# Kernel optimization log

Hardware: AMD Instinct MI355X
Metric: run time of the kernel (lower is better)

The kernel has to match this reference:

```python
import jax, jax.numpy as jnp
import numpy as np

N = 100000
F_IN = 128
HID = 128
E = 1600000


def gcn_conv(x, W, b, src, dst, dinv):
    # PyG GCNConv: h = x @ W; out_i = sum_j norm_ij * h_j (incl. self-loop) + b
    h = x @ W  # [N, H]
    norm = dinv[src] * dinv[dst]  # [E]
    msg = h[src] * norm[:, None]  # [E, H]
    agg = jax.ops.segment_sum(msg, dst, num_segments=N)
    agg = agg + h * (dinv * dinv)[:, None]  # self-loop contribution
    return agg + b


def setup_inputs() -> dict:
    key = jax.random.key(0)
    k1, k2, k3, k4, k5 = jax.random.split(key, 5)
    x = jax.random.normal(k1, (N, F_IN), dtype=jnp.float32)
    edge_index = jax.random.randint(k2, (2, E), 0, N, dtype=jnp.int64)
    s = 1.0 / np.sqrt(F_IN)
    W1 = jax.random.normal(k3, (F_IN, HID), dtype=jnp.float32) * s
    b1 = jnp.zeros((HID,), dtype=jnp.float32)
    sh = 1.0 / np.sqrt(HID)
    W2 = jax.random.normal(k4, (HID, HID), dtype=jnp.float32) * sh
    b2 = jnp.zeros((HID,), dtype=jnp.float32)
    Wfc = jax.random.normal(k5, (HID, 2), dtype=jnp.float32) * sh
    bfc = jnp.zeros((2,), dtype=jnp.float32)
    return {"x": x, "edge_index": edge_index, "W1": W1, "b1": b1,
            "W2": W2, "b2": b2, "Wfc": Wfc, "bfc": bfc}


def reference(x, edge_index, W1, b1, W2, b2, Wfc, bfc):
    src, dst = edge_index[0], edge_index[1]
    # degree with self-loops (edge weight 1), computed on target nodes
    deg = jax.ops.segment_sum(jnp.ones((E,), jnp.float32), dst, num_segments=N) + 1.0
    dinv = jax.lax.rsqrt(deg)
    h = jax.nn.relu(gcn_conv(x, W1, b1, src, dst, dinv))
    h = jax.nn.relu(gcn_conv(h, W2, b2, src, dst, dinv))
    logits = h @ Wfc + bfc  # [N, 2]
    return jax.nn.log_softmax(logits, axis=1)
```

## Files before the change

kernel.cpp:

```cpp
#include <hip/hip_runtime.h>
#include <math.h>

#define N_NODES 100000
#define FDIM 128
#define E_EDGES 1600000
#define NSCAN_BLKS ((N_NODES + 1023) / 1024)
#define NPASS 8
#define PASS_NODES 12500

typedef unsigned short bf16_t;
typedef __attribute__((ext_vector_type(8))) short short8;
typedef __attribute__((ext_vector_type(4))) float f32x4;

__device__ inline bf16_t f2bf(float f) {
    unsigned int u = __float_as_uint(f);
    return (bf16_t)((u + 0x7fffu + ((u >> 16) & 1u)) >> 16);
}
__device__ inline float2 bfpair(unsigned int u) {
    return make_float2(__uint_as_float(u << 16), __uint_as_float(u & 0xffff0000u));
}

__global__ __launch_bounds__(256) void hist_kernel(const int* __restrict__ dst,
                                                   int* __restrict__ cnt) {
    int pass = blockIdx.x & (NPASS - 1);
    int e = (blockIdx.x >> 3) * 256 + threadIdx.x;
    if (e >= E_EDGES) return;
    int d = dst[e];
    if ((unsigned)(d - pass * PASS_NODES) < (unsigned)PASS_NODES)
        atomicAdd(&cnt[d], 1);
}

__global__ __launch_bounds__(256) void scan1(const int* __restrict__ cnt,
                                             int* __restrict__ excl,
                                             int* __restrict__ bsum) {
    __shared__ int lds[256];
    const int b = blockIdx.x, t = threadIdx.x;
    const int base = b * 1024 + t * 4;
    int v[4];
#pragma unroll
    for (int q = 0; q < 4; ++q) {
        int i = base + q;
        v[q] = (i < N_NODES) ? cnt[i] : 0;
    }
    int tsum = v[0] + v[1] + v[2] + v[3];
    lds[t] = tsum;
    __syncthreads();
    for (int off = 1; off < 256; off <<= 1) {
        int x = lds[t];
        int y = (t >= off) ? lds[t - off] : 0;
        __syncthreads();
        lds[t] = x + y;
        __syncthreads();
    }
    int texcl = lds[t] - tsum;
    if (t == 255) bsum[b] = lds[t];
    int run = texcl;
#pragma unroll
    for (int q = 0; q < 4; ++q) {
        int i = base + q;
        if (i < N_NODES) excl[i] = run;
        run += v[q];
    }
}

__global__ __launch_bounds__(128) void scan2(int* __restrict__ bsum) {
    __shared__ int lds[128];
    const int t = threadIdx.x;
    int v = (t < NSCAN_BLKS) ? bsum[t] : 0;
    lds[t] = v;
    __syncthreads();
    for (int off = 1; off < 128; off <<= 1) {
        int x = lds[t];
        int y = (t >= off) ? lds[t - off] : 0;
        __syncthreads();
        lds[t] = x + y;
        __syncthreads();
    }
    if (t < NSCAN_BLKS) bsum[t] = lds[t] - v;
}

__global__ __launch_bounds__(256) void scan3(int* __restrict__ rowptr,
                                             const int* __restrict__ bsum,
                                             const int* __restrict__ cnt,
                                             float* __restrict__ dinv) {
    int i = blockIdx.x * blockDim.x + threadIdx.x;
    if (i < N_NODES) {
        rowptr[i] += bsum[i >> 10];
        dinv[i] = rsqrtf((float)cnt[i] + 1.0f);
    }
    if (i == 0) rowptr[N_NODES] = E_EDGES;
}

__global__ __launch_bounds__(256) void scatter_kernel(const int* __restrict__ src,
                                                      const int* __restrict__ dst,
                                                      const int* __restrict__ rowptr,
                                                      const float* __restrict__ dinv,
                                                      int* __restrict__ cursor,
                                                      int2* __restrict__ emeta) {
    int pass = blockIdx.x & (NPASS - 1);
    int e = (blockIdx.x >> 3) * 256 + threadIdx.x;
    if (e >= E_EDGES) return;
    int d = dst[e];
    if ((unsigned)(d - pass * PASS_NODES) < (unsigned)PASS_NODES) {
        int s = src[e];
        int p = rowptr[d] + atomicAdd(&cursor[d], 1);
        float nrm = dinv[s] * dinv[d];
        emeta[p] = make_int2(s, __float_as_int(nrm));
    }
}

__global__ __launch_bounds__(256) void wcvt_kernel(const float* __restrict__ W,
                                                   bf16_t* __restrict__ Wt) {
    int idx = blockIdx.x * 256 + threadIdx.x;
    int k = idx >> 7, c = idx & 127;
    Wt[c * 128 + k] = f2bf(W[idx]);
}

template <bool A_IS_F32>
__global__ __launch_bounds__(256) void gemm_mfma(const void* __restrict__ Aptr,
                                                 const bf16_t* __restrict__ Wt,
                                                 bf16_t* __restrict__ H) {
    const int tid = threadIdx.x;
    const int wave = tid >> 6;
    const int l = tid & 63;
    const int r = l & 15;
    const int g = l >> 4;
    const int row0 = (blockIdx.x * 4 + wave) * 16;
    const int arow = min(row0 + r, N_NODES - 1);

    f32x4 acc[8];
#pragma unroll
    for (int ct = 0; ct < 8; ++ct) acc[ct] = (f32x4){0.f, 0.f, 0.f, 0.f};

#pragma unroll
    for (int ks = 0; ks < 4; ++ks) {
        const int kbase = ks * 32 + g * 8;
        short8 a;
        if constexpr (A_IS_F32) {
            const float* X = (const float*)Aptr;
            const float4 x0 = *((const float4*)(X + (size_t)arow * 128 + kbase));
            const float4 x1 = *((const float4*)(X + (size_t)arow * 128 + kbase + 4));
            a[0] = (short)f2bf(x0.x); a[1] = (short)f2bf(x0.y);
            a[2] = (short)f2bf(x0.z); a[3] = (short)f2bf(x0.w);
            a[4] = (short)f2bf(x1.x); a[5] = (short)f2bf(x1.y);
            a[6] = (short)f2bf(x1.z); a[7] = (short)f2bf(x1.w);
        } else {
            const bf16_t* X = (const bf16_t*)Aptr;
            a = *((const short8*)(X + (size_t)arow * 128 + kbase));
        }
#pragma unroll
        for (int ct = 0; ct < 8; ++ct) {
            short8 b = *((const short8*)(Wt + (ct * 16 + r) * 128 + kbase));
            acc[ct] = __builtin_amdgcn_mfma_f32_16x16x32_bf16(a, b, acc[ct], 0, 0, 0);
        }
    }

#pragma unroll
    for (int j = 0; j < 4; ++j) {
        const int row = row0 + g * 4 + j;
        if (row < N_NODES) {
            bf16_t* hp = H + (size_t)row * 128 + r;
#pragma unroll
            for (int ct = 0; ct < 8; ++ct) hp[ct * 16] = f2bf(acc[ct][j]);
        }
    }
}

__global__ __launch_bounds__(256) void agg_kernel(const int* __restrict__ rowptr,
                                                  const int2* __restrict__ emeta,
                                                  const float* __restrict__ dinv,
                                                  const bf16_t* __restrict__ h,
                                                  const float* __restrict__ bias,
                                                  bf16_t* __restrict__ out) {
    int gid = blockIdx.x * blockDim.x + threadIdx.x;
    int node = gid >> 6;
    int lane = gid & 63;
    if (node >= N_NODES) return;
    float dd = dinv[node];
    float2 v = bfpair(((const unsigned*)(h + (size_t)node * 128))[lane]);
    float sc = dd * dd;
    float accx = v.x * sc, accy = v.y * sc;
    int j = rowptr[node];
    const int end = rowptr[node + 1];
    for (; j + 3 < end; j += 4) {
        int2 m0 = emeta[j], m1 = emeta[j + 1], m2 = emeta[j + 2], m3 = emeta[j + 3];
        float n0 = __int_as_float(m0.y), n1 = __int_as_float(m1.y);
        float n2 = __int_as_float(m2.y), n3 = __int_as_float(m3.y);
        float2 v0 = bfpair(((const unsigned*)(h + (size_t)m0.x * 128))[lane]);
        float2 v1 = bfpair(((const unsigned*)(h + (size_t)m1.x * 128))[lane]);
        float2 v2 = bfpair(((const unsigned*)(h + (size_t)m2.x * 128))[lane]);
        float2 v3 = bfpair(((const unsigned*)(h + (size_t)m3.x * 128))[lane]);
        accx += v0.x * n0 + v1.x * n1 + v2.x * n2 + v3.x * n3;
        accy += v0.y * n0 + v1.y * n1 + v2.y * n2 + v3.y * n3;
    }
    for (; j < end; ++j) {
        int2 m0 = emeta[j];
        float n0 = __int_as_float(m0.y);
        float2 v0 = bfpair(((const unsigned*)(h + (size_t)m0.x * 128))[lane]);
        accx += v0.x * n0;
        accy += v0.y * n0;
    }
    float2 b = ((const float2*)bias)[lane];
    accx = fmaxf(accx + b.x, 0.f);
    accy = fmaxf(accy + b.y, 0.f);
    unsigned o = (unsigned)f2bf(accx) | ((unsigned)f2bf(accy) << 16);
    ((unsigned*)(out + (size_t)node * 128))[lane] = o;
}

__global__ __launch_bounds__(256) void agg_fc_kernel(const int* __restrict__ rowptr,
                                                     const int2* __restrict__ emeta,
                                                     const float* __restrict__ dinv,
                                                     const bf16_t* __restrict__ h,
                                                     const float* __restrict__ bias,
                                                     const float* __restrict__ Wfc,
                                                     const float* __restrict__ bfc,
                                                     float* __restrict__ out) {
    int gid = blockIdx.x * blockDim.x + threadIdx.x;
    int node = gid >> 6;
    int lane = gid & 63;
    if (node >= N_NODES) return;
    float dd = dinv[node];
    float2 v = bfpair(((const unsigned*)(h + (size_t)node * 128))[lane]);
    float sc = dd * dd;
    float accx = v.x * sc, accy = v.y * sc;
    int j = rowptr[node];
    const int end = rowptr[node + 1];
    for (; j + 3 < end; j += 4) {
        int2 m0 = emeta[j], m1 = emeta[j + 1], m2 = emeta[j + 2], m3 = emeta[j + 3];
        float n0 = __int_as_float(m0.y), n1 = __int_as_float(m1.y);
        float n2 = __int_as_float(m2.y), n3 = __int_as_float(m3.y);
        float2 v0 = bfpair(((const unsigned*)(h + (size_t)m0.x * 128))[lane]);
        float2 v1 = bfpair(((const unsigned*)(h + (size_t)m1.x * 128))[lane]);
        float2 v2 = bfpair(((const unsigned*)(h + (size_t)m2.x * 128))[lane]);
        float2 v3 = bfpair(((const unsigned*)(h + (size_t)m3.x * 128))[lane]);
        accx += v0.x * n0 + v1.x * n1 + v2.x * n2 + v3.x * n3;
        accy += v0.y * n0 + v1.y * n1 + v2.y * n2 + v3.y * n3;
    }
    for (; j < end; ++j) {
        int2 m0 = emeta[j];
        float n0 = __int_as_float(m0.y);
        float2 v0 = bfpair(((const unsigned*)(h + (size_t)m0.x * 128))[lane]);
        accx += v0.x * n0;
        accy += v0.y * n0;
    }
    float2 b = ((const float2*)bias)[lane];
    accx = fmaxf(accx + b.x, 0.f);
    accy = fmaxf(accy + b.y, 0.f);
    int k0 = lane * 2;
    float a0 = accx * Wfc[k0 * 2 + 0] + accy * Wfc[(k0 + 1) * 2 + 0];
    float a1 = accx * Wfc[k0 * 2 + 1] + accy * Wfc[(k0 + 1) * 2 + 1];
#pragma unroll
    for (int off = 32; off > 0; off >>= 1) {
        a0 += __shfl_down(a0, off);
        a1 += __shfl_down(a1, off);
    }
    if (lane == 0) {
        float l0 = a0 + bfc[0];
        float l1 = a1 + bfc[1];
        float m = fmaxf(l0, l1);
        float lse = m + logf(expf(l0 - m) + expf(l1 - m));
        out[(size_t)node * 2 + 0] = l0 - lse;
        out[(size_t)node * 2 + 1] = l1 - lse;
    }
}

extern "C" void kernel_launch(void* const* d_in, const int* in_sizes, int n_in,
                              void* d_out, int out_size, void* d_ws, size_t ws_size,
                              hipStream_t stream) {
    const float* x   = (const float*)d_in[0];
    const int*   ei  = (const int*)d_in[1];
    const float* W1  = (const float*)d_in[2];
    const float* b1  = (const float*)d_in[3];
    const float* W2  = (const float*)d_in[4];
    const float* b2  = (const float*)d_in[5];
    const float* Wfc = (const float*)d_in[6];
    const float* bfc = (const float*)d_in[7];
    float* out = (float*)d_out;

    const int* src = ei;
    const int* dst = ei + E_EDGES;

    char* wp = (char*)d_ws;
    auto carve = [&](size_t bytes) -> char* {
        char* p = wp;
        wp += (bytes + 255) & ~(size_t)255;
        return p;
    };
    int*    cnt    = (int*)carve(N_NODES * 4);
    int*    rowptr = (int*)carve((N_NODES + 1) * 4);
    int*    cursor = (int*)carve(N_NODES * 4);
    int*    bsum   = (int*)carve(128 * 4);
    int2*   emeta  = (int2*)carve((size_t)E_EDGES * 8);
    float*  dinv   = (float*)carve(N_NODES * 4);
    bf16_t* hbuf   = (bf16_t*)carve((size_t)N_NODES * FDIM * 2);
    bf16_t* x2buf  = (bf16_t*)carve((size_t)N_NODES * FDIM * 2);
    bf16_t* Wt1    = (bf16_t*)carve(128 * 128 * 2);
    bf16_t* Wt2    = (bf16_t*)carve(128 * 128 * 2);

    const int NN_BLK = (N_NODES + 255) / 256;
    const int NODE_WAVE_BLK = (N_NODES * 64 + 255) / 256;
    const int EDGE_PASS_BLK = ((E_EDGES + 255) / 256) * NPASS;
    const int GEMM_BLK = (N_NODES + 63) / 64;

    hipMemsetAsync(cnt, 0, N_NODES * sizeof(int), stream);
    hipMemsetAsync(cursor, 0, N_NODES * sizeof(int), stream);
    hist_kernel<<<EDGE_PASS_BLK, 256, 0, stream>>>(dst, cnt);
    scan1<<<NSCAN_BLKS, 256, 0, stream>>>(cnt, rowptr, bsum);
    scan2<<<1, 128, 0, stream>>>(bsum);
    scan3<<<NN_BLK, 256, 0, stream>>>(rowptr, bsum, cnt, dinv);
    scatter_kernel<<<EDGE_PASS_BLK, 256, 0, stream>>>(src, dst, rowptr, dinv,
                                                      cursor, emeta);

    wcvt_kernel<<<64, 256, 0, stream>>>(W1, Wt1);
    wcvt_kernel<<<64, 256, 0, stream>>>(W2, Wt2);

    gemm_mfma<true><<<GEMM_BLK, 256, 0, stream>>>(x, Wt1, hbuf);
    agg_kernel<<<NODE_WAVE_BLK, 256, 0, stream>>>(rowptr, emeta, dinv, hbuf, b1, x2buf);

    gemm_mfma<false><<<GEMM_BLK, 256, 0, stream>>>(x2buf, Wt2, hbuf);
    agg_fc_kernel<<<NODE_WAVE_BLK, 256, 0, stream>>>(rowptr, emeta, dinv, hbuf, b2,
                                                     Wfc, bfc, out);
}
```

Baseline: 470.2 us.

## Prefetch edge metadata in aggregation, double GEMM rows per wave, merge small launches

```diff
diff --git a/kernel.cpp b/kernel.cpp
--- a/kernel.cpp
+++ b/kernel.cpp
@@ -82,11 +82,13 @@
 __global__ __launch_bounds__(256) void scan3(int* __restrict__ rowptr,
                                              const int* __restrict__ bsum,
                                              const int* __restrict__ cnt,
-                                             float* __restrict__ dinv) {
+                                             float* __restrict__ dinv,
+                                             int* __restrict__ cursor) {
     int i = blockIdx.x * blockDim.x + threadIdx.x;
     if (i < N_NODES) {
         rowptr[i] += bsum[i >> 10];
         dinv[i] = rsqrtf((float)cnt[i] + 1.0f);
+        cursor[i] = 0;
     }
     if (i == 0) rowptr[N_NODES] = E_EDGES;
 }
@@ -109,9 +111,14 @@
     }
 }
 
-__global__ __launch_bounds__(256) void wcvt_kernel(const float* __restrict__ W,
-                                                   bf16_t* __restrict__ Wt) {
-    int idx = blockIdx.x * 256 + threadIdx.x;
+__global__ __launch_bounds__(256) void wcvt_kernel(const float* __restrict__ W1,
+                                                   bf16_t* __restrict__ Wt1,
+                                                   const float* __restrict__ W2,
+                                                   bf16_t* __restrict__ Wt2) {
+    int gid = blockIdx.x * 256 + threadIdx.x;
+    const float* W = (gid < 16384) ? W1 : W2;
+    bf16_t* Wt = (gid < 16384) ? Wt1 : Wt2;
+    int idx = gid & 16383;
     int k = idx >> 7, c = idx & 127;
     Wt[c * 128 + k] = f2bf(W[idx]);
 }
@@ -125,43 +132,61 @@
     const int l = tid & 63;
     const int r = l & 15;
     const int g = l >> 4;
-    const int row0 = (blockIdx.x * 4 + wave) * 16;
-    const int arow = min(row0 + r, N_NODES - 1);
-
-    f32x4 acc[8];
-#pragma unroll
-    for (int ct = 0; ct < 8; ++ct) acc[ct] = (f32x4){0.f, 0.f, 0.f, 0.f};
+    const int rowbase = (blockIdx.x * 8 + wave * 2) * 16;
+    const int arow0 = min(rowbase + r, N_NODES - 1);
+    const int arow1 = min(rowbase + 16 + r, N_NODES - 1);
+
+    f32x4 acc0[8], acc1[8];
+#pragma unroll
+    for (int ct = 0; ct < 8; ++ct) {
+        acc0[ct] = (f32x4){0.f, 0.f, 0.f, 0.f};
+        acc1[ct] = (f32x4){0.f, 0.f, 0.f, 0.f};
+    }
 
 #pragma unroll
     for (int ks = 0; ks < 4; ++ks) {
         const int kbase = ks * 32 + g * 8;
-        short8 a;
+        short8 a0, a1;
         if constexpr (A_IS_F32) {
             const float* X = (const float*)Aptr;
-            const float4 x0 = *((const float4*)(X + (size_t)arow * 128 + kbase));
-            const float4 x1 = *((const float4*)(X + (size_t)arow * 128 + kbase + 4));
-            a[0] = (short)f2bf(x0.x); a[1] = (short)f2bf(x0.y);
-            a[2] = (short)f2bf(x0.z); a[3] = (short)f2bf(x0.w);
-            a[4] = (short)f2bf(x1.x); a[5] = (short)f2bf(x1.y);
-            a[6] = (short)f2bf(x1.z); a[7] = (short)f2bf(x1.w);
+            const float4 p0 = *((const float4*)(X + (size_t)arow0 * 128 + kbase));
+            const float4 p1 = *((const float4*)(X + (size_t)arow0 * 128 + kbase + 4));
+            const float4 q0 = *((const float4*)(X + (size_t)arow1 * 128 + kbase));
+            const float4 q1 = *((const float4*)(X + (size_t)arow1 * 128 + kbase + 4));
+            a0[0] = (short)f2bf(p0.x); a0[1] = (short)f2bf(p0.y);
+            a0[2] = (short)f2bf(p0.z); a0[3] = (short)f2bf(p0.w);
+            a0[4] = (short)f2bf(p1.x); a0[5] = (short)f2bf(p1.y);
+            a0[6] = (short)f2bf(p1.z); a0[7] = (short)f2bf(p1.w);
+            a1[0] = (short)f2bf(q0.x); a1[1] = (short)f2bf(q0.y);
+            a1[2] = (short)f2bf(q0.z); a1[3] = (short)f2bf(q0.w);
+            a1[4] = (short)f2bf(q1.x); a1[5] = (short)f2bf(q1.y);
+            a1[6] = (short)f2bf(q1.z); a1[7] = (short)f2bf(q1.w);
         } else {
             const bf16_t* X = (const bf16_t*)Aptr;
-            a = *((const short8*)(X + (size_t)arow * 128 + kbase));
+            a0 = *((const short8*)(X + (size_t)arow0 * 128 + kbase));
+            a1 = *((const short8*)(X + (size_t)arow1 * 128 + kbase));
         }
 #pragma unroll
         for (int ct = 0; ct < 8; ++ct) {
             short8 b = *((const short8*)(Wt + (ct * 16 + r) * 128 + kbase));
-            acc[ct] = __builtin_amdgcn_mfma_f32_16x16x32_bf16(a, b, acc[ct], 0, 0, 0);
+            acc0[ct] = __builtin_amdgcn_mfma_f32_16x16x32_bf16(a0, b, acc0[ct], 0, 0, 0);
+            acc1[ct] = __builtin_amdgcn_mfma_f32_16x16x32_bf16(a1, b, acc1[ct], 0, 0, 0);
         }
     }
 
 #pragma unroll
     for (int j = 0; j < 4; ++j) {
-        const int row = row0 + g * 4 + j;
-        if (row < N_NODES) {
-            bf16_t* hp = H + (size_t)row * 128 + r;
-#pragma unroll
-            for (int ct = 0; ct < 8; ++ct) hp[ct * 16] = f2bf(acc[ct][j]);
+        const int row0 = rowbase + g * 4 + j;
+        if (row0 < N_NODES) {
+            bf16_t* hp = H + (size_t)row0 * 128 + r;
+#pragma unroll
+            for (int ct = 0; ct < 8; ++ct) hp[ct * 16] = f2bf(acc0[ct][j]);
+        }
+        const int row1 = rowbase + 16 + g * 4 + j;
+        if (row1 < N_NODES) {
+            bf16_t* hp = H + (size_t)row1 * 128 + r;
+#pragma unroll
+            for (int ct = 0; ct < 8; ++ct) hp[ct * 16] = f2bf(acc1[ct][j]);
         }
     }
 }
@@ -176,35 +201,66 @@
     int node = gid >> 6;
     int lane = gid & 63;
     if (node >= N_NODES) return;
+    const unsigned* __restrict__ hu = (const unsigned*)h;
+
     float dd = dinv[node];
-    float2 v = bfpair(((const unsigned*)(h + (size_t)node * 128))[lane]);
+    float2 v = bfpair(hu[(size_t)node * 64 + lane]);
     float sc = dd * dd;
     float accx = v.x * sc, accy = v.y * sc;
+
     int j = rowptr[node];
     const int end = rowptr[node + 1];
-    for (; j + 3 < end; j += 4) {
-        int2 m0 = emeta[j], m1 = emeta[j + 1], m2 = emeta[j + 2], m3 = emeta[j + 3];
-        float n0 = __int_as_float(m0.y), n1 = __int_as_float(m1.y);
-        float n2 = __int_as_float(m2.y), n3 = __int_as_float(m3.y);
-        float2 v0 = bfpair(((const unsigned*)(h + (size_t)m0.x * 128))[lane]);
-        float2 v1 = bfpair(((const unsigned*)(h + (size_t)m1.x * 128))[lane]);
-        float2 v2 = bfpair(((const unsigned*)(h + (size_t)m2.x * 128))[lane]);
-        float2 v3 = bfpair(((const unsigned*)(h + (size_t)m3.x * 128))[lane]);
-        accx += v0.x * n0 + v1.x * n1 + v2.x * n2 + v3.x * n3;
-        accy += v0.y * n0 + v1.y * n1 + v2.y * n2 + v3.y * n3;
+
+    int2 m0, m1, m2, m3, m4, m5, m6, m7;
+    bool have = (j + 8 <= end);
+    if (have) {
+        m0 = emeta[j + 0]; m1 = emeta[j + 1]; m2 = emeta[j + 2]; m3 = emeta[j + 3];
+        m4 = emeta[j + 4]; m5 = emeta[j + 5]; m6 = emeta[j + 6]; m7 = emeta[j + 7];
+    }
+    while (have) {
+        const int jn = j + 8;
+        const bool nxt = (jn + 8 <= end);
+        int2 t0, t1, t2, t3, t4, t5, t6, t7;
+        if (nxt) {
+            t0 = emeta[jn + 0]; t1 = emeta[jn + 1]; t2 = emeta[jn + 2]; t3 = emeta[jn + 3];
+            t4 = emeta[jn + 4]; t5 = emeta[jn + 5]; t6 = emeta[jn + 6]; t7 = emeta[jn + 7];
+        }
+        float2 v0 = bfpair(hu[(size_t)m0.x * 64 + lane]);
+        float2 v1 = bfpair(hu[(size_t)m1.x * 64 + lane]);
+        float2 v2 = bfpair(hu[(size_t)m2.x * 64 + lane]);
+        float2 v3 = bfpair(hu[(size_t)m3.x * 64 + lane]);
+        float2 v4 = bfpair(hu[(size_t)m4.x * 64 + lane]);
+        float2 v5 = bfpair(hu[(size_t)m5.x * 64 + lane]);
+        float2 v6 = bfpair(hu[(size_t)m6.x * 64 + lane]);
+        float2 v7 = bfpair(hu[(size_t)m7.x * 64 + lane]);
+        accx += v0.x * __int_as_float(m0.y) + v1.x * __int_as_float(m1.y)
+              + v2.x * __int_as_float(m2.y) + v3.x * __int_as_float(m3.y)
+              + v4.x * __int_as_float(m4.y) + v5.x * __int_as_float(m5.y)
+              + v6.x * __int_as_float(m6.y) + v7.x * __int_as_float(m7.y);
+        accy += v0.y * __int_as_float(m0.y) + v1.y * __int_as_float(m1.y)
+              + v2.y * __int_as_float(m2.y) + v3.y * __int_as_float(m3.y)
+              + v4.y * __int_as_float(m4.y) + v5.y * __int_as_float(m5.y)
+              + v6.y * __int_as_float(m6.y) + v7.y * __int_as_float(m7.y);
+        j = jn;
+        have = nxt;
+        if (nxt) {
+            m0 = t0; m1 = t1; m2 = t2; m3 = t3;
+            m4 = t4; m5 = t5; m6 = t6; m7 = t7;
+        }
     }
     for (; j < end; ++j) {
-        int2 m0 = emeta[j];
-        float n0 = __int_as_float(m0.y);
-        float2 v0 = bfpair(((const unsigned*)(h + (size_t)m0.x * 128))[lane]);
+        int2 m = emeta[j];
+        float2 v0 = bfpair(hu[(size_t)m.x * 64 + lane]);
+        float n0 = __int_as_float(m.y);
         accx += v0.x * n0;
         accy += v0.y * n0;
     }
+
     float2 b = ((const float2*)bias)[lane];
     accx = fmaxf(accx + b.x, 0.f);
     accy = fmaxf(accy + b.y, 0.f);
     unsigned o = (unsigned)f2bf(accx) | ((unsigned)f2bf(accy) << 16);
-    ((unsigned*)(out + (size_t)node * 128))[lane] = o;
+    ((unsigned*)out)[(size_t)node * 64 + lane] = o;
 }
 
 __global__ __launch_bounds__(256) void agg_fc_kernel(const int* __restrict__ rowptr,
@@ -219,30 +275,61 @@
     int node = gid >> 6;
     int lane = gid & 63;
     if (node >= N_NODES) return;
+    const unsigned* __restrict__ hu = (const unsigned*)h;
+
     float dd = dinv[node];
-    float2 v = bfpair(((const unsigned*)(h + (size_t)node * 128))[lane]);
+    float2 v = bfpair(hu[(size_t)node * 64 + lane]);
     float sc = dd * dd;
     float accx = v.x * sc, accy = v.y * sc;
+
     int j = rowptr[node];
     const int end = rowptr[node + 1];
-    for (; j + 3 < end; j += 4) {
-        int2 m0 = emeta[j], m1 = emeta[j + 1], m2 = emeta[j + 2], m3 = emeta[j + 3];
-        float n0 = __int_as_float(m0.y), n1 = __int_as_float(m1.y);
-        float n2 = __int_as_float(m2.y), n3 = __int_as_float(m3.y);
-        float2 v0 = bfpair(((const unsigned*)(h + (size_t)m0.x * 128))[lane]);
-        float2 v1 = bfpair(((const unsigned*)(h + (size_t)m1.x * 128))[lane]);
-        float2 v2 = bfpair(((const unsigned*)(h + (size_t)m2.x * 128))[lane]);
-        float2 v3 = bfpair(((const unsigned*)(h + (size_t)m3.x * 128))[lane]);
-        accx += v0.x * n0 + v1.x * n1 + v2.x * n2 + v3.x * n3;
-        accy += v0.y * n0 + v1.y * n1 + v2.y * n2 + v3.y * n3;
+
+    int2 m0, m1, m2, m3, m4, m5, m6, m7;
+    bool have = (j + 8 <= end);
+    if (have) {
+        m0 = emeta[j + 0]; m1 = emeta[j + 1]; m2 = emeta[j + 2]; m3 = emeta[j + 3];
+        m4 = emeta[j + 4]; m5 = emeta[j + 5]; m6 = emeta[j + 6]; m7 = emeta[j + 7];
+    }
+    while (have) {
+        const int jn = j + 8;
+        const bool nxt = (jn + 8 <= end);
+        int2 t0, t1, t2, t3, t4, t5, t6, t7;
+        if (nxt) {
+            t0 = emeta[jn + 0]; t1 = emeta[jn + 1]; t2 = emeta[jn + 2]; t3 = emeta[jn + 3];
+            t4 = emeta[jn + 4]; t5 = emeta[jn + 5]; t6 = emeta[jn + 6]; t7 = emeta[jn + 7];
+        }
+        float2 v0 = bfpair(hu[(size_t)m0.x * 64 + lane]);
+        float2 v1 = bfpair(hu[(size_t)m1.x * 64 + lane]);
+        float2 v2 = bfpair(hu[(size_t)m2.x * 64 + lane]);
+        float2 v3 = bfpair(hu[(size_t)m3.x * 64 + lane]);
+        float2 v4 = bfpair(hu[(size_t)m4.x * 64 + lane]);
+        float2 v5 = bfpair(hu[(size_t)m5.x * 64 + lane]);
+        float2 v6 = bfpair(hu[(size_t)m6.x * 64 + lane]);
+        float2 v7 = bfpair(hu[(size_t)m7.x * 64 + lane]);
+        accx += v0.x * __int_as_float(m0.y) + v1.x * __int_as_float(m1.y)
+              + v2.x * __int_as_float(m2.y) + v3.x * __int_as_float(m3.y)
+              + v4.x * __int_as_float(m4.y) + v5.x * __int_as_float(m5.y)
+              + v6.x * __int_as_float(m6.y) + v7.x * __int_as_float(m7.y);
+        accy += v0.y * __int_as_float(m0.y) + v1.y * __int_as_float(m1.y)
+              + v2.y * __int_as_float(m2.y) + v3.y * __int_as_float(m3.y)
+              + v4.y * __int_as_float(m4.y) + v5.y * __int_as_float(m5.y)
+              + v6.y * __int_as_float(m6.y) + v7.y * __int_as_float(m7.y);
+        j = jn;
+        have = nxt;
+        if (nxt) {
+            m0 = t0; m1 = t1; m2 = t2; m3 = t3;
+            m4 = t4; m5 = t5; m6 = t6; m7 = t7;
+        }
     }
     for (; j < end; ++j) {
-        int2 m0 = emeta[j];
-        float n0 = __int_as_float(m0.y);
-        float2 v0 = bfpair(((const unsigned*)(h + (size_t)m0.x * 128))[lane]);
+        int2 m = emeta[j];
+        float2 v0 = bfpair(hu[(size_t)m.x * 64 + lane]);
+        float n0 = __int_as_float(m.y);
         accx += v0.x * n0;
         accy += v0.y * n0;
     }
+
     float2 b = ((const float2*)bias)[lane];
     accx = fmaxf(accx + b.x, 0.f);
     accy = fmaxf(accy + b.y, 0.f);
@@ -300,19 +387,17 @@
     const int NN_BLK = (N_NODES + 255) / 256;
     const int NODE_WAVE_BLK = (N_NODES * 64 + 255) / 256;
     const int EDGE_PASS_BLK = ((E_EDGES + 255) / 256) * NPASS;
-    const int GEMM_BLK = (N_NODES + 63) / 64;
+    const int GEMM_BLK = (N_NODES + 127) / 128;
 
     hipMemsetAsync(cnt, 0, N_NODES * sizeof(int), stream);
-    hipMemsetAsync(cursor, 0, N_NODES * sizeof(int), stream);
     hist_kernel<<<EDGE_PASS_BLK, 256, 0, stream>>>(dst, cnt);
     scan1<<<NSCAN_BLKS, 256, 0, stream>>>(cnt, rowptr, bsum);
     scan2<<<1, 128, 0, stream>>>(bsum);
-    scan3<<<NN_BLK, 256, 0, stream>>>(rowptr, bsum, cnt, dinv);
+    scan3<<<NN_BLK, 256, 0, stream>>>(rowptr, bsum, cnt, dinv, cursor);
     scatter_kernel<<<EDGE_PASS_BLK, 256, 0, stream>>>(src, dst, rowptr, dinv,
                                                       cursor, emeta);
 
-    wcvt_kernel<<<64, 256, 0, stream>>>(W1, Wt1);
-    wcvt_kernel<<<64, 256, 0, stream>>>(W2, Wt2);
+    wcvt_kernel<<<128, 256, 0, stream>>>(W1, Wt1, W2, Wt2);
 
     gemm_mfma<true><<<GEMM_BLK, 256, 0, stream>>>(x, Wt1, hbuf);
     agg_kernel<<<NODE_WAVE_BLK, 256, 0, stream>>>(rowptr, emeta, dinv, hbuf, b1, x2buf);
```

Measured after the change: 456.0 us. 1.03x faster.
